# Kernel optimization log

Measured on AMD Instinct MI355X. Metric: run time of the kernel, lower is better.

The kernel has to match this reference:

```python
import jax, jax.numpy as jnp
import numpy as np


def _avgpool2(x):
    # 2x2 average pool, stride 2, NHWC
    B, H, W, C = x.shape
    return x.reshape(B, H // 2, 2, W // 2, 2, C).mean(axis=(2, 4))


def setup_inputs() -> dict:
    key = jax.random.key(0)
    ks = jax.random.split(key, 5)
    B, H, W, C = 8, 64, 64, 512
    s = 0.02
    return {
        "x": jax.random.normal(ks[0], (B, H, W, C), dtype=jnp.float32),
        "wf": jax.random.normal(ks[1], (C, C // 8), dtype=jnp.float32) * s,
        "wg": jax.random.normal(ks[2], (C, C // 8), dtype=jnp.float32) * s,
        "wh": jax.random.normal(ks[3], (C, C // 2), dtype=jnp.float32) * s,
        "wo": jax.random.normal(ks[4], (C // 2, C), dtype=jnp.float32) * s,
    }


def reference(x, wf, wg, wh, wo):
    B, H, W, C = x.shape
    # queries from full resolution: 1x1 conv == channel matmul
    f = jnp.einsum("bhwc,cd->bhwd", x, wf).reshape(B, H * W, C // 8)
    # keys/values from 2x2 average-pooled map
    xp = _avgpool2(x)  # [B, H/2, W/2, C]
    g = jnp.einsum("bhwc,cd->bhwd", xp, wg).reshape(B, H * W // 4, C // 8)
    h = jnp.einsum("bhwc,cd->bhwd", xp, wh).reshape(B, H * W // 4, C // 2)
    # attn: [B, HW, HW/4], softmax over pooled key axis
    attn = jax.nn.softmax(jnp.einsum("bnd,bmd->bnm", f, g), axis=-1)
    y = jnp.einsum("bnm,bmd->bnd", attn, h).reshape(B, H, W, C // 2)
    # output 1x1 conv back to C channels
    return jnp.einsum("bhwc,cd->bhwd", y, wo)
```

## Files before the change

kernel.cpp:

```cpp
#include <hip/hip_runtime.h>
#include <hip/hip_bf16.h>

typedef __attribute__((ext_vector_type(8))) short bshort8;
typedef __attribute__((ext_vector_type(4))) float f32x4;
typedef __attribute__((ext_vector_type(4))) float vfloat4;
typedef __attribute__((ext_vector_type(4))) unsigned int vuint4;
typedef __attribute__((ext_vector_type(2))) unsigned int vuint2;

__device__ __forceinline__ unsigned short f2bf(float f) {
    union { float f; unsigned u; } v; v.f = f;
    unsigned u = v.u;
    u += 0x7fffu + ((u >> 16) & 1u);
    return (unsigned short)(u >> 16);
}

template<int EPI, bool AF32>
__global__ __launch_bounds__(256)
void gemm_bt(const void* __restrict__ Av, const unsigned short* __restrict__ Btv,
             void* __restrict__ Cv,
             int M, int N, int K)
{
    __shared__ __align__(128) char sA[64 * 64];
    __shared__ __align__(128) char sB[64 * 64];

    const int tid  = threadIdx.x;
    const int bRow = blockIdx.y << 6;
    const int bCol = blockIdx.x << 6;
    const int wid  = tid >> 6, lane = tid & 63;
    const int wr   = wid >> 1, wc   = wid & 1;
    const int r16  = lane & 15, kg  = lane >> 4;
    const int srow = tid >> 2,  skc = tid & 3;

    f32x4 acc[2][2] = {};

    const size_t aRowBase = (size_t)(bRow + srow) * K + skc * 8;
    const size_t bRowBase = (size_t)(bCol + srow) * K + skc * 8;
    const unsigned swW = ((((unsigned)srow) << 6) | (((unsigned)skc) << 4))
                         ^ ((((unsigned)srow) & 7u) << 4);

    for (int k0 = 0; k0 < K; k0 += 32) {
        vuint4 apack;
        if constexpr (AF32) {
            const float* ap = (const float*)Av + aRowBase + k0;
            vfloat4 x0 = *(const vfloat4*)ap;
            vfloat4 x1 = *(const vfloat4*)(ap + 4);
            apack[0] = (unsigned)f2bf(x0[0]) | ((unsigned)f2bf(x0[1]) << 16);
            apack[1] = (unsigned)f2bf(x0[2]) | ((unsigned)f2bf(x0[3]) << 16);
            apack[2] = (unsigned)f2bf(x1[0]) | ((unsigned)f2bf(x1[1]) << 16);
            apack[3] = (unsigned)f2bf(x1[2]) | ((unsigned)f2bf(x1[3]) << 16);
        } else {
            const unsigned short* ap = (const unsigned short*)Av + aRowBase + k0;
            apack = *(const vuint4*)ap;
        }
        vuint4 bpack = *(const vuint4*)((const unsigned short*)Btv + bRowBase + k0);
        *(vuint4*)(sA + swW) = apack;
        *(vuint4*)(sB + swW) = bpack;
        __syncthreads();

        bshort8 af[2], bfr[2];
        #pragma unroll
        for (int mi = 0; mi < 2; mi++) {
            unsigned row = (unsigned)(wr * 32 + mi * 16 + r16);
            unsigned off = ((row << 6) | (((unsigned)kg) << 4)) ^ ((row & 7u) << 4);
            af[mi] = *(const bshort8*)(sA + off);
        }
        #pragma unroll
        for (int ni = 0; ni < 2; ni++) {
            unsigned col = (unsigned)(wc * 32 + ni * 16 + r16);
            unsigned off = ((col << 6) | (((unsigned)kg) << 4)) ^ ((col & 7u) << 4);
            bfr[ni] = *(const bshort8*)(sB + off);
        }
        #pragma unroll
        for (int mi = 0; mi < 2; mi++)
            #pragma unroll
            for (int ni = 0; ni < 2; ni++)
                acc[mi][ni] = __builtin_amdgcn_mfma_f32_16x16x32_bf16(
                                  af[mi], bfr[ni], acc[mi][ni], 0, 0, 0);
        __syncthreads();
    }

    #pragma unroll
    for (int mi = 0; mi < 2; mi++) {
        const int row0 = bRow + wr * 32 + mi * 16 + kg * 4;
        #pragma unroll
        for (int ni = 0; ni < 2; ni++) {
            const int col = bCol + wc * 32 + ni * 16 + r16;
            #pragma unroll
            for (int r = 0; r < 4; r++) {
                const int row = row0 + r;
                float x = acc[mi][ni][r];
                const size_t ci = (size_t)row * N + col;
                if constexpr (EPI == 0) ((float*)Cv)[ci] = x;
                else                    ((unsigned short*)Cv)[ci] = f2bf(x);
            }
        }
    }
}

__global__ __launch_bounds__(256)
void flash_attn(const unsigned short* __restrict__ fb,
                const unsigned short* __restrict__ gb,
                const unsigned short* __restrict__ ht,
                unsigned short* __restrict__ yb)
{
    __shared__ __align__(128) char sS[64 * 128];
    __shared__ __align__(128) char sG[64 * 128];
    __shared__ __align__(128) char sH[256 * 128];
    __shared__ float rs[64];

    const int tid = threadIdx.x;
    const int b   = blockIdx.y;
    const int q0  = blockIdx.x << 6;
    const int wid = tid >> 6, lane = tid & 63;
    const int wr  = wid >> 1, wc = wid & 1;
    const int r16 = lane & 15, kg = lane >> 4;

    const unsigned short* fB = fb + ((size_t)b * 4096 + q0) * 64;
    const unsigned short* gB = gb + (size_t)b * 1024 * 64;
    const unsigned short* hB = ht + (size_t)b * 256 * 1024;

    {
        const int row = tid >> 2, kc0 = tid & 3;
        #pragma unroll
        for (int it = 0; it < 2; it++) {
            const int kc = kc0 + it * 4;
            vuint4 v = *(const vuint4*)(fB + (size_t)row * 64 + kc * 8);
            unsigned off = ((unsigned)row * 128 + (unsigned)kc * 16) ^ (((unsigned)row & 7u) << 4);
            *(vuint4*)(sS + off) = v;
        }
    }
    __syncthreads();

    bshort8 af[2][2];
    #pragma unroll
    for (int mi = 0; mi < 2; mi++)
        #pragma unroll
        for (int s = 0; s < 2; s++) {
            unsigned row = (unsigned)(wr * 32 + mi * 16 + r16);
            unsigned off = (row * 128 + (unsigned)s * 64 + (unsigned)kg * 16) ^ ((row & 7u) << 4);
            af[mi][s] = *(const bshort8*)(sS + off);
        }

    f32x4 yacc[2][8] = {};
    float psum[2][4] = {};

    const int kc = tid & 7, n0 = tid >> 3;

    for (int c = 0; c < 16; c++) {
        const int kv0 = c << 6;
        #pragma unroll
        for (int it = 0; it < 2; it++) {
            const int n = n0 + it * 32;
            vuint4 v = *(const vuint4*)(gB + (size_t)(kv0 + n) * 64 + kc * 8);
            unsigned off = ((unsigned)n * 128 + (unsigned)kc * 16) ^ (((unsigned)n & 7u) << 4);
            *(vuint4*)(sG + off) = v;
        }
        #pragma unroll
        for (int it = 0; it < 8; it++) {
            const int n = n0 + it * 32;
            vuint4 v = *(const vuint4*)(hB + (size_t)n * 1024 + kv0 + kc * 8);
            unsigned off = ((unsigned)n * 128 + (unsigned)kc * 16) ^ (((unsigned)n & 7u) << 4);
            *(vuint4*)(sH + off) = v;
        }
        __syncthreads();

        f32x4 sacc[2][2] = {};
        #pragma unroll
        for (int ni = 0; ni < 2; ni++)
            #pragma unroll
            for (int s = 0; s < 2; s++) {
                unsigned col = (unsigned)(wc * 32 + ni * 16 + r16);
                unsigned off = (col * 128 + (unsigned)s * 64 + (unsigned)kg * 16) ^ ((col & 7u) << 4);
                bshort8 g8 = *(const bshort8*)(sG + off);
                #pragma unroll
                for (int mi = 0; mi < 2; mi++)
                    sacc[mi][ni] = __builtin_amdgcn_mfma_f32_16x16x32_bf16(
                                       af[mi][s], g8, sacc[mi][ni], 0, 0, 0);
            }

        #pragma unroll
        for (int mi = 0; mi < 2; mi++)
            #pragma unroll
            for (int ni = 0; ni < 2; ni++) {
                const unsigned col = (unsigned)(wc * 32 + ni * 16 + r16);
                #pragma unroll
                for (int r = 0; r < 4; r++) {
                    float e = __expf(sacc[mi][ni][r]);
                    psum[mi][r] += e;
                    unsigned row = (unsigned)(wr * 32 + mi * 16 + kg * 4 + r);
                    unsigned off = (row * 128 + col * 2) ^ ((row & 7u) << 4);
                    *(unsigned short*)(sS + off) = f2bf(e);
                }
            }
        __syncthreads();

        bshort8 pa[2][2];
        #pragma unroll
        for (int mi = 0; mi < 2; mi++)
            #pragma unroll
            for (int s = 0; s < 2; s++) {
                unsigned row = (unsigned)(wr * 32 + mi * 16 + r16);
                unsigned off = (row * 128 + (unsigned)s * 64 + (unsigned)kg * 16) ^ ((row & 7u) << 4);
                pa[mi][s] = *(const bshort8*)(sS + off);
            }
        #pragma unroll
        for (int ni = 0; ni < 8; ni++) {
            unsigned col = (unsigned)(wc * 128 + ni * 16 + r16);
            unsigned base = col * 128;
            unsigned sw = (col & 7u) << 4;
            bshort8 b0 = *(const bshort8*)(sH + ((base + (unsigned)kg * 16) ^ sw));
            bshort8 b1 = *(const bshort8*)(sH + ((base + 64 + (unsigned)kg * 16) ^ sw));
            #pragma unroll
            for (int mi = 0; mi < 2; mi++) {
                yacc[mi][ni] = __builtin_amdgcn_mfma_f32_16x16x32_bf16(pa[mi][0], b0, yacc[mi][ni], 0, 0, 0);
                yacc[mi][ni] = __builtin_amdgcn_mfma_f32_16x16x32_bf16(pa[mi][1], b1, yacc[mi][ni], 0, 0, 0);
            }
        }
        __syncthreads();
    }

    #pragma unroll
    for (int mi = 0; mi < 2; mi++)
        #pragma unroll
        for (int r = 0; r < 4; r++) {
            float s = psum[mi][r];
            s += __shfl_xor(s, 1, 64);
            s += __shfl_xor(s, 2, 64);
            s += __shfl_xor(s, 4, 64);
            s += __shfl_xor(s, 8, 64);
            psum[mi][r] = s;
        }
    if (wc == 0 && r16 == 0) {
        #pragma unroll
        for (int mi = 0; mi < 2; mi++)
            #pragma unroll
            for (int r = 0; r < 4; r++)
                rs[wr * 32 + mi * 16 + kg * 4 + r] = psum[mi][r];
    }
    __syncthreads();
    if (wc == 1 && r16 == 0) {
        #pragma unroll
        for (int mi = 0; mi < 2; mi++)
            #pragma unroll
            for (int r = 0; r < 4; r++)
                rs[wr * 32 + mi * 16 + kg * 4 + r] += psum[mi][r];
    }
    __syncthreads();

    unsigned short* yB = yb + ((size_t)b * 4096 + q0) * 256;
    #pragma unroll
    for (int mi = 0; mi < 2; mi++)
        #pragma unroll
        for (int r = 0; r < 4; r++) {
            const int row = wr * 32 + mi * 16 + kg * 4 + r;
            const float rinv = 1.0f / rs[row];
            #pragma unroll
            for (int ni = 0; ni < 8; ni++) {
                const int col = wc * 128 + ni * 16 + r16;
                yB[(size_t)row * 256 + col] = f2bf(yacc[mi][ni][r] * rinv);
            }
        }
}

__global__ __launch_bounds__(256)
void pool2(const float* __restrict__ x, unsigned short* __restrict__ xp)
{
    const int t  = blockIdx.x * 256 + threadIdx.x;
    const int c4 = t & 127;
    const int j  = (t >> 7) & 31;
    const int i  = (t >> 12) & 31;
    const int b  = t >> 17;
    const float* p = x + ((((size_t)b * 64 + 2 * i) * 64) + 2 * j) * 512 + c4 * 4;
    vfloat4 a0 = *(const vfloat4*)p;
    vfloat4 a1 = *(const vfloat4*)(p + 512);
    vfloat4 a2 = *(const vfloat4*)(p + 64 * 512);
    vfloat4 a3 = *(const vfloat4*)(p + 64 * 512 + 512);
    float r0 = 0.25f * (a0[0] + a1[0] + a2[0] + a3[0]);
    float r1 = 0.25f * (a0[1] + a1[1] + a2[1] + a3[1]);
    float r2 = 0.25f * (a0[2] + a1[2] + a2[2] + a3[2]);
    float r3 = 0.25f * (a0[3] + a1[3] + a2[3] + a3[3]);
    vuint2 o;
    o[0] = (unsigned)f2bf(r0) | ((unsigned)f2bf(r1) << 16);
    o[1] = (unsigned)f2bf(r2) | ((unsigned)f2bf(r3) << 16);
    *(vuint2*)(xp + (size_t)t * 4) = o;
}

__global__ __launch_bounds__(256)
void transpose_cast(const float* __restrict__ in, unsigned short* __restrict__ out,
                    int Kdim, int Ndim)
{
    const int idx = blockIdx.x * 256 + threadIdx.x;
    if (idx >= Kdim * Ndim) return;
    const int n = idx / Kdim, k = idx % Kdim;
    out[idx] = f2bf(in[(size_t)k * Ndim + n]);
}

__global__ __launch_bounds__(256)
void transpose_h(const unsigned short* __restrict__ h, unsigned short* __restrict__ ht)
{
    __shared__ unsigned short tile[32][33];
    const int b  = blockIdx.z;
    const int v0 = blockIdx.x * 32, m0 = blockIdx.y * 32;
    const int tx = threadIdx.x & 31, ty = threadIdx.x >> 5;
    const unsigned short* hp = h + (size_t)b * 1024 * 256;
    #pragma unroll
    for (int s = 0; s < 4; s++)
        tile[ty + s * 8][tx] = hp[(size_t)(m0 + ty + s * 8) * 256 + v0 + tx];
    __syncthreads();
    unsigned short* op = ht + (size_t)b * 256 * 1024;
    #pragma unroll
    for (int s = 0; s < 4; s++)
        op[(size_t)(v0 + ty + s * 8) * 1024 + m0 + tx] = tile[tx][ty + s * 8];
}

extern "C" void kernel_launch(void* const* d_in, const int* in_sizes, int n_in,
                              void* d_out, int out_size, void* d_ws, size_t ws_size,
                              hipStream_t stream)
{
    const float* x  = (const float*)d_in[0];
    const float* wf = (const float*)d_in[1];
    const float* wg = (const float*)d_in[2];
    const float* wh = (const float*)d_in[3];
    const float* wo = (const float*)d_in[4];
    float* out = (float*)d_out;

    char* ws = (char*)d_ws;
    size_t off = 0;
    auto carve = [&](size_t bytes) {
        char* p = ws + off;
        off = (off + bytes + 255) & ~(size_t)255;
        return p;
    };
    unsigned short* xp   = (unsigned short*)carve(8ll * 1024 * 512 * 2);
    unsigned short* wf_t = (unsigned short*)carve(64 * 512 * 2);
    unsigned short* wg_t = (unsigned short*)carve(64 * 512 * 2);
    unsigned short* wh_t = (unsigned short*)carve(256 * 512 * 2);
    unsigned short* wo_t = (unsigned short*)carve(512 * 256 * 2);
    unsigned short* fb   = (unsigned short*)carve(8ll * 4096 * 64 * 2);
    unsigned short* gb   = (unsigned short*)carve(8ll * 1024 * 64 * 2);
    unsigned short* hb   = (unsigned short*)carve(8ll * 1024 * 256 * 2);
    unsigned short* ht   = (unsigned short*)carve(8ll * 256 * 1024 * 2);
    unsigned short* yb   = (unsigned short*)carve(8ll * 4096 * 256 * 2);

    transpose_cast<<<dim3(128),  256, 0, stream>>>(wf, wf_t, 512, 64);
    transpose_cast<<<dim3(128),  256, 0, stream>>>(wg, wg_t, 512, 64);
    transpose_cast<<<dim3(512),  256, 0, stream>>>(wh, wh_t, 512, 256);
    transpose_cast<<<dim3(512),  256, 0, stream>>>(wo, wo_t, 256, 512);

    pool2<<<dim3(4096), 256, 0, stream>>>(x, xp);

    gemm_bt<1, true ><<<dim3(1, 512, 1), 256, 0, stream>>>(x,  wf_t, fb, 32768, 64, 512);
    gemm_bt<1, false><<<dim3(1, 128, 1), 256, 0, stream>>>(xp, wg_t, gb, 8192, 64, 512);
    gemm_bt<1, false><<<dim3(4, 128, 1), 256, 0, stream>>>(xp, wh_t, hb, 8192, 256, 512);
    transpose_h<<<dim3(8, 32, 8), 256, 0, stream>>>(hb, ht);

    flash_attn<<<dim3(64, 8), 256, 0, stream>>>(fb, gb, ht, yb);

    gemm_bt<0, false><<<dim3(8, 512, 1), 256, 0, stream>>>(yb, wo_t, out, 32768, 512, 256);
}
```

Measured before the change: 219.9 us.

## Fuse query projection into attention kernel and halve query tile per block

The separate f = x·wf GEMM launch and its bf16 intermediate buffer are removed. The attention kernel now loads fp32 x rows, casts them to bf16, and computes the 32-row query tile with MFMA before the attention loop. The query tile per block drops from 64 to 32 rows, so the grid grows to 1024 blocks, which raises parallelism. In exchange, each block reloads the full G and H key/value tiles for half as many queries, doubling that traffic.

```diff
diff --git a/kernel.cpp b/kernel.cpp
--- a/kernel.cpp
+++ b/kernel.cpp
@@ -14,9 +14,9 @@
     return (unsigned short)(u >> 16);
 }
 
-template<int EPI, bool AF32>
-__global__ __launch_bounds__(256)
-void gemm_bt(const void* __restrict__ Av, const unsigned short* __restrict__ Btv,
+template<int EPI>
+__global__ __launch_bounds__(256)
+void gemm_bt(const unsigned short* __restrict__ Av, const unsigned short* __restrict__ Btv,
              void* __restrict__ Cv,
              int M, int N, int K)
 {
@@ -39,20 +39,8 @@
                          ^ ((((unsigned)srow) & 7u) << 4);
 
     for (int k0 = 0; k0 < K; k0 += 32) {
-        vuint4 apack;
-        if constexpr (AF32) {
-            const float* ap = (const float*)Av + aRowBase + k0;
-            vfloat4 x0 = *(const vfloat4*)ap;
-            vfloat4 x1 = *(const vfloat4*)(ap + 4);
-            apack[0] = (unsigned)f2bf(x0[0]) | ((unsigned)f2bf(x0[1]) << 16);
-            apack[1] = (unsigned)f2bf(x0[2]) | ((unsigned)f2bf(x0[3]) << 16);
-            apack[2] = (unsigned)f2bf(x1[0]) | ((unsigned)f2bf(x1[1]) << 16);
-            apack[3] = (unsigned)f2bf(x1[2]) | ((unsigned)f2bf(x1[3]) << 16);
-        } else {
-            const unsigned short* ap = (const unsigned short*)Av + aRowBase + k0;
-            apack = *(const vuint4*)ap;
-        }
-        vuint4 bpack = *(const vuint4*)((const unsigned short*)Btv + bRowBase + k0);
+        vuint4 apack = *(const vuint4*)(Av + aRowBase + k0);
+        vuint4 bpack = *(const vuint4*)(Btv + bRowBase + k0);
         *(vuint4*)(sA + swW) = apack;
         *(vuint4*)(sB + swW) = bpack;
         __syncthreads();
@@ -98,52 +86,98 @@
 }
 
 __global__ __launch_bounds__(256)
-void flash_attn(const unsigned short* __restrict__ fb,
+void flash_attn(const float* __restrict__ x,
+                const unsigned short* __restrict__ wft,
                 const unsigned short* __restrict__ gb,
                 const unsigned short* __restrict__ ht,
                 unsigned short* __restrict__ yb)
 {
-    __shared__ __align__(128) char sS[64 * 128];
+    __shared__ __align__(128) char sS[32 * 128];
     __shared__ __align__(128) char sG[64 * 128];
     __shared__ __align__(128) char sH[256 * 128];
-    __shared__ float rs[64];
+    __shared__ float rs[32];
 
     const int tid = threadIdx.x;
-    const int b   = blockIdx.y;
-    const int q0  = blockIdx.x << 6;
+    const int bid = blockIdx.x;
+    const int b   = bid & 7;
+    const int q0  = (bid >> 3) << 5;
     const int wid = tid >> 6, lane = tid & 63;
     const int wr  = wid >> 1, wc = wid & 1;
     const int r16 = lane & 15, kg = lane >> 4;
 
-    const unsigned short* fB = fb + ((size_t)b * 4096 + q0) * 64;
+    const float*          xB = x  + ((size_t)b * 4096 + q0) * 512;
     const unsigned short* gB = gb + (size_t)b * 1024 * 64;
     const unsigned short* hB = ht + (size_t)b * 256 * 1024;
 
+    f32x4 facc[2] = {};
     {
-        const int row = tid >> 2, kc0 = tid & 3;
-        #pragma unroll
-        for (int it = 0; it < 2; it++) {
-            const int kc = kc0 + it * 4;
-            vuint4 v = *(const vuint4*)(fB + (size_t)row * 64 + kc * 8);
-            unsigned off = ((unsigned)row * 128 + (unsigned)kc * 16) ^ (((unsigned)row & 7u) << 4);
-            *(vuint4*)(sS + off) = v;
+        const int xrow = tid >> 3, xc8 = tid & 7;
+        const int wrow = tid >> 2, wk0 = tid & 3;
+        for (int k0 = 0; k0 < 512; k0 += 64) {
+            {
+                const float* p = xB + (size_t)xrow * 512 + k0 + xc8 * 8;
+                vfloat4 a0 = *(const vfloat4*)p;
+                vfloat4 a1 = *(const vfloat4*)(p + 4);
+                vuint4 w;
+                w[0] = (unsigned)f2bf(a0[0]) | ((unsigned)f2bf(a0[1]) << 16);
+                w[1] = (unsigned)f2bf(a0[2]) | ((unsigned)f2bf(a0[3]) << 16);
+                w[2] = (unsigned)f2bf(a1[0]) | ((unsigned)f2bf(a1[1]) << 16);
+                w[3] = (unsigned)f2bf(a1[2]) | ((unsigned)f2bf(a1[3]) << 16);
+                unsigned off = ((unsigned)xrow * 128 + (unsigned)xc8 * 16)
+                               ^ (((unsigned)xrow & 7u) << 4);
+                *(vuint4*)(sH + off) = w;
+            }
+            #pragma unroll
+            for (int it = 0; it < 2; it++) {
+                const int skc = wk0 + it * 4;
+                vuint4 v = *(const vuint4*)(wft + (size_t)wrow * 512 + k0 + skc * 8);
+                unsigned off = ((unsigned)wrow * 128 + (unsigned)skc * 16)
+                               ^ (((unsigned)wrow & 7u) << 4);
+                *(vuint4*)(sG + off) = v;
+            }
+            __syncthreads();
+
+            bshort8 ax0, ax1;
+            {
+                unsigned row = (unsigned)(wr * 16 + r16);
+                unsigned base = row * 128, sw = (row & 7u) << 4;
+                ax0 = *(const bshort8*)(sH + ((base + (unsigned)kg * 16) ^ sw));
+                ax1 = *(const bshort8*)(sH + ((base + 64 + (unsigned)kg * 16) ^ sw));
+            }
+            #pragma unroll
+            for (int ni = 0; ni < 2; ni++) {
+                unsigned col = (unsigned)(wc * 32 + ni * 16 + r16);
+                unsigned base = col * 128, sw = (col & 7u) << 4;
+                bshort8 b0 = *(const bshort8*)(sG + ((base + (unsigned)kg * 16) ^ sw));
+                bshort8 b1 = *(const bshort8*)(sG + ((base + 64 + (unsigned)kg * 16) ^ sw));
+                facc[ni] = __builtin_amdgcn_mfma_f32_16x16x32_bf16(ax0, b0, facc[ni], 0, 0, 0);
+                facc[ni] = __builtin_amdgcn_mfma_f32_16x16x32_bf16(ax1, b1, facc[ni], 0, 0, 0);
+            }
+            __syncthreads();
+        }
+    }
+
+    #pragma unroll
+    for (int ni = 0; ni < 2; ni++) {
+        const unsigned col = (unsigned)(wc * 32 + ni * 16 + r16);
+        #pragma unroll
+        for (int r = 0; r < 4; r++) {
+            unsigned row = (unsigned)(wr * 16 + kg * 4 + r);
+            unsigned off = (row * 128 + col * 2) ^ ((row & 7u) << 4);
+            *(unsigned short*)(sS + off) = f2bf(facc[ni][r]);
         }
     }
     __syncthreads();
-
-    bshort8 af[2][2];
-    #pragma unroll
-    for (int mi = 0; mi < 2; mi++)
-        #pragma unroll
-        for (int s = 0; s < 2; s++) {
-            unsigned row = (unsigned)(wr * 32 + mi * 16 + r16);
-            unsigned off = (row * 128 + (unsigned)s * 64 + (unsigned)kg * 16) ^ ((row & 7u) << 4);
-            af[mi][s] = *(const bshort8*)(sS + off);
-        }
-
-    f32x4 yacc[2][8] = {};
-    float psum[2][4] = {};
-
+    bshort8 af[2];
+    {
+        unsigned row = (unsigned)(wr * 16 + r16);
+        unsigned base = row * 128, sw = (row & 7u) << 4;
+        af[0] = *(const bshort8*)(sS + ((base + (unsigned)kg * 16) ^ sw));
+        af[1] = *(const bshort8*)(sS + ((base + 64 + (unsigned)kg * 16) ^ sw));
+    }
+
+    f32x4 yacc[8] = {};
+    float psum[4] = {};
     const int kc = tid & 7, n0 = tid >> 3;
 
     for (int c = 0; c < 16; c++) {
@@ -164,102 +198,83 @@
         }
         __syncthreads();
 
-        f32x4 sacc[2][2] = {};
-        #pragma unroll
-        for (int ni = 0; ni < 2; ni++)
-            #pragma unroll
-            for (int s = 0; s < 2; s++) {
-                unsigned col = (unsigned)(wc * 32 + ni * 16 + r16);
-                unsigned off = (col * 128 + (unsigned)s * 64 + (unsigned)kg * 16) ^ ((col & 7u) << 4);
-                bshort8 g8 = *(const bshort8*)(sG + off);
-                #pragma unroll
-                for (int mi = 0; mi < 2; mi++)
-                    sacc[mi][ni] = __builtin_amdgcn_mfma_f32_16x16x32_bf16(
-                                       af[mi][s], g8, sacc[mi][ni], 0, 0, 0);
-            }
-
-        #pragma unroll
-        for (int mi = 0; mi < 2; mi++)
-            #pragma unroll
-            for (int ni = 0; ni < 2; ni++) {
-                const unsigned col = (unsigned)(wc * 32 + ni * 16 + r16);
-                #pragma unroll
-                for (int r = 0; r < 4; r++) {
-                    float e = __expf(sacc[mi][ni][r]);
-                    psum[mi][r] += e;
-                    unsigned row = (unsigned)(wr * 32 + mi * 16 + kg * 4 + r);
-                    unsigned off = (row * 128 + col * 2) ^ ((row & 7u) << 4);
-                    *(unsigned short*)(sS + off) = f2bf(e);
-                }
-            }
-        __syncthreads();
-
-        bshort8 pa[2][2];
-        #pragma unroll
-        for (int mi = 0; mi < 2; mi++)
-            #pragma unroll
-            for (int s = 0; s < 2; s++) {
-                unsigned row = (unsigned)(wr * 32 + mi * 16 + r16);
-                unsigned off = (row * 128 + (unsigned)s * 64 + (unsigned)kg * 16) ^ ((row & 7u) << 4);
-                pa[mi][s] = *(const bshort8*)(sS + off);
-            }
+        f32x4 sacc[2] = {};
+        #pragma unroll
+        for (int ni = 0; ni < 2; ni++) {
+            unsigned col = (unsigned)(wc * 32 + ni * 16 + r16);
+            unsigned base = col * 128, sw = (col & 7u) << 4;
+            bshort8 g0 = *(const bshort8*)(sG + ((base + (unsigned)kg * 16) ^ sw));
+            bshort8 g1 = *(const bshort8*)(sG + ((base + 64 + (unsigned)kg * 16) ^ sw));
+            sacc[ni] = __builtin_amdgcn_mfma_f32_16x16x32_bf16(af[0], g0, sacc[ni], 0, 0, 0);
+            sacc[ni] = __builtin_amdgcn_mfma_f32_16x16x32_bf16(af[1], g1, sacc[ni], 0, 0, 0);
+        }
+
+        #pragma unroll
+        for (int ni = 0; ni < 2; ni++) {
+            const unsigned col = (unsigned)(wc * 32 + ni * 16 + r16);
+            #pragma unroll
+            for (int r = 0; r < 4; r++) {
+                float e = __expf(sacc[ni][r]);
+                psum[r] += e;
+                unsigned row = (unsigned)(wr * 16 + kg * 4 + r);
+                unsigned off = (row * 128 + col * 2) ^ ((row & 7u) << 4);
+                *(unsigned short*)(sS + off) = f2bf(e);
+            }
+        }
+        __syncthreads();
+
+        bshort8 pa0, pa1;
+        {
+            unsigned row = (unsigned)(wr * 16 + r16);
+            unsigned base = row * 128, sw = (row & 7u) << 4;
+            pa0 = *(const bshort8*)(sS + ((base + (unsigned)kg * 16) ^ sw));
+            pa1 = *(const bshort8*)(sS + ((base + 64 + (unsigned)kg * 16) ^ sw));
+        }
         #pragma unroll
         for (int ni = 0; ni < 8; ni++) {
             unsigned col = (unsigned)(wc * 128 + ni * 16 + r16);
-            unsigned base = col * 128;
-            unsigned sw = (col & 7u) << 4;
+            unsigned base = col * 128, sw = (col & 7u) << 4;
             bshort8 b0 = *(const bshort8*)(sH + ((base + (unsigned)kg * 16) ^ sw));
             bshort8 b1 = *(const bshort8*)(sH + ((base + 64 + (unsigned)kg * 16) ^ sw));
-            #pragma unroll
-            for (int mi = 0; mi < 2; mi++) {
-                yacc[mi][ni] = __builtin_amdgcn_mfma_f32_16x16x32_bf16(pa[mi][0], b0, yacc[mi][ni], 0, 0, 0);
-                yacc[mi][ni] = __builtin_amdgcn_mfma_f32_16x16x32_bf16(pa[mi][1], b1, yacc[mi][ni], 0, 0, 0);
-            }
-        }
-        __syncthreads();
-    }
-
-    #pragma unroll
-    for (int mi = 0; mi < 2; mi++)
-        #pragma unroll
-        for (int r = 0; r < 4; r++) {
-            float s = psum[mi][r];
-            s += __shfl_xor(s, 1, 64);
-            s += __shfl_xor(s, 2, 64);
-            s += __shfl_xor(s, 4, 64);
-            s += __shfl_xor(s, 8, 64);
-            psum[mi][r] = s;
-        }
+            yacc[ni] = __builtin_amdgcn_mfma_f32_16x16x32_bf16(pa0, b0, yacc[ni], 0, 0, 0);
+            yacc[ni] = __builtin_amdgcn_mfma_f32_16x16x32_bf16(pa1, b1, yacc[ni], 0, 0, 0);
+        }
+        __syncthreads();
+    }
+
+    #pragma unroll
+    for (int r = 0; r < 4; r++) {
+        float s = psum[r];
+        s += __shfl_xor(s, 1, 64);
+        s += __shfl_xor(s, 2, 64);
+        s += __shfl_xor(s, 4, 64);
+        s += __shfl_xor(s, 8, 64);
+        psum[r] = s;
+    }
     if (wc == 0 && r16 == 0) {
         #pragma unroll
-        for (int mi = 0; mi < 2; mi++)
-            #pragma unroll
-            for (int r = 0; r < 4; r++)
-                rs[wr * 32 + mi * 16 + kg * 4 + r] = psum[mi][r];
+        for (int r = 0; r < 4; r++)
+            rs[wr * 16 + kg * 4 + r] = psum[r];
     }
     __syncthreads();
     if (wc == 1 && r16 == 0) {
         #pragma unroll
-        for (int mi = 0; mi < 2; mi++)
-            #pragma unroll
-            for (int r = 0; r < 4; r++)
-                rs[wr * 32 + mi * 16 + kg * 4 + r] += psum[mi][r];
+        for (int r = 0; r < 4; r++)
+            rs[wr * 16 + kg * 4 + r] += psum[r];
     }
     __syncthreads();
 
     unsigned short* yB = yb + ((size_t)b * 4096 + q0) * 256;
     #pragma unroll
-    for (int mi = 0; mi < 2; mi++)
-        #pragma unroll
-        for (int r = 0; r < 4; r++) {
-            const int row = wr * 32 + mi * 16 + kg * 4 + r;
-            const float rinv = 1.0f / rs[row];
-            #pragma unroll
-            for (int ni = 0; ni < 8; ni++) {
-                const int col = wc * 128 + ni * 16 + r16;
-                yB[(size_t)row * 256 + col] = f2bf(yacc[mi][ni][r] * rinv);
-            }
-        }
+    for (int r = 0; r < 4; r++) {
+        const int row = wr * 16 + kg * 4 + r;
+        const float rinv = 1.0f / rs[row];
+        #pragma unroll
+        for (int ni = 0; ni < 8; ni++) {
+            const int col = wc * 128 + ni * 16 + r16;
+            yB[(size_t)row * 256 + col] = f2bf(yacc[ni][r] * rinv);
+        }
+    }
 }
 
 __global__ __launch_bounds__(256)
@@ -336,7 +351,6 @@
     unsigned short* wg_t = (unsigned short*)carve(64 * 512 * 2);
     unsigned short* wh_t = (unsigned short*)carve(256 * 512 * 2);
     unsigned short* wo_t = (unsigned short*)carve(512 * 256 * 2);
-    unsigned short* fb   = (unsigned short*)carve(8ll * 4096 * 64 * 2);
     unsigned short* gb   = (unsigned short*)carve(8ll * 1024 * 64 * 2);
     unsigned short* hb   = (unsigned short*)carve(8ll * 1024 * 256 * 2);
     unsigned short* ht   = (unsigned short*)carve(8ll * 256 * 1024 * 2);
@@ -349,12 +363,11 @@
 
     pool2<<<dim3(4096), 256, 0, stream>>>(x, xp);
 
-    gemm_bt<1, true ><<<dim3(1, 512, 1), 256, 0, stream>>>(x,  wf_t, fb, 32768, 64, 512);
-    gemm_bt<1, false><<<dim3(1, 128, 1), 256, 0, stream>>>(xp, wg_t, gb, 8192, 64, 512);
-    gemm_bt<1, false><<<dim3(4, 128, 1), 256, 0, stream>>>(xp, wh_t, hb, 8192, 256, 512);
+    gemm_bt<1><<<dim3(1, 128, 1), 256, 0, stream>>>(xp, wg_t, gb, 8192, 64, 512);
+    gemm_bt<1><<<dim3(4, 128, 1), 256, 0, stream>>>(xp, wh_t, hb, 8192, 256, 512);
     transpose_h<<<dim3(8, 32, 8), 256, 0, stream>>>(hb, ht);
 
-    flash_attn<<<dim3(64, 8), 256, 0, stream>>>(fb, gb, ht, yb);
-
-    gemm_bt<0, false><<<dim3(8, 512, 1), 256, 0, stream>>>(yb, wo_t, out, 32768, 512, 256);
-}
+    flash_attn<<<dim3(1024), 256, 0, stream>>>(x, wf_t, gb, ht, yb);
+
+    gemm_bt<0><<<dim3(8, 512, 1), 256, 0, stream>>>(yb, wo_t, out, 32768, 512, 256);
+}
```

New measurement: 300.4 us. 36.6% more time.
